# Optimization experiments

Measured on AMD Instinct MI355X. Metric: run time of the kernel, lower is better.

## Reference

```python
import jax, jax.numpy as jnp
import numpy as np

LMAX = 4
NC = (LMAX + 1) ** 2          # 25 spherical coefficients
L0 = LMAX + 1                 # number of m=0 coefficients
SPHERE = 128
CIN1 = 2 * SPHERE             # concat(source, target) channels
HID = 64
HEADS = 8
ALPHA_C = 64
VAL_C = 16
OUT_C = 128
GRID = 2 * (LMAX + 1)         # S2 grid resolution
N_NODES = 2500
N_EDGES = 25000
MAX_ELEM = 90
EDGE_IN = 128 + 2 * 64        # distance basis + src/tgt atom embeddings
M_SIZES = [LMAX - m + 1 for m in range(1, LMAX + 1)]  # l-count per |m|>0
RAD_OUT = L0 * CIN1 + sum(s * CIN1 for s in M_SIZES)  # 3840

def _lm(l, m):
    return l * l + l + m
_p = [_lm(l, 0) for l in range(LMAX + 1)]
for m in range(1, LMAX + 1):
    _p += [_lm(l, -m) for l in range(m, LMAX + 1)]
    _p += [_lm(l, m) for l in range(m, LMAX + 1)]
PERM = np.asarray(_p)             # l-primary -> m-primary
INV_PERM = np.argsort(PERM)       # m-primary -> l-primary
EXPAND = np.concatenate([np.full(2 * l + 1, l) for l in range(LMAX + 1)])

def _layernorm(x, g, b, eps=1e-5):
    mu = jnp.mean(x, axis=-1, keepdims=True)
    var = jnp.mean((x - mu) ** 2, axis=-1, keepdims=True)
    return (x - mu) * jax.lax.rsqrt(var + eps) * g + b

def _so2_conv(xm, fc0_w, fc0_b, wms, cin, mout, extra, rad):
    # xm: [E, NC, cin] in m-primary layout. Per-order SO(2) 'complex' conv.
    E = xm.shape[0]
    x0 = xm[:, :L0].reshape(E, L0 * cin)
    off_rad = L0 * cin
    if rad is not None:
        x0 = x0 * rad[:, :off_rad]
    x0 = x0 @ fc0_w + fc0_b
    x0_extra = None
    if extra:
        x0_extra = x0[:, :extra]
        x0 = x0[:, extra:]
    outs = [x0.reshape(E, L0, mout)]
    off = L0
    for i, sz in enumerate(M_SIZES):
        xb = xm[:, off:off + 2 * sz].reshape(E, 2, sz * cin)
        if rad is not None:
            xb = xb * rad[:, off_rad:off_rad + sz * cin][:, None, :]
            off_rad += sz * cin
        y = xb @ wms[i]                         # [E, 2, 2*mout*sz]
        half = y.shape[-1] // 2
        yr, yi = y[..., :half], y[..., half:]
        o = jnp.stack([yr[:, 0] - yi[:, 1], yr[:, 1] + yi[:, 0]], axis=1)
        outs.append(o.reshape(E, 2 * sz, mout))
        off += 2 * sz
    return jnp.concatenate(outs, axis=1), x0_extra

def _segment_softmax(logits, seg, num_segments):
    mx = jax.ops.segment_max(logits, seg, num_segments=num_segments)
    ex = jnp.exp(logits - mx[seg])
    s = jax.ops.segment_sum(ex, seg, num_segments=num_segments)
    return ex / (s[seg] + 1e-16)

def setup_inputs():
    key = jax.random.key(0)
    ks = iter(jax.random.split(key, 64))
    def nrm(shape, scale=1.0):
        return jax.random.normal(next(ks), shape, dtype=jnp.float32) * scale
    def lin(i, o):
        return nrm((i, o), i ** -0.5)
    inp = {}
    inp['x'] = nrm((N_NODES, NC, SPHERE))
    inp['edge_distance'] = nrm((N_EDGES, 128))
    inp['src_table'] = jax.random.uniform(next(ks), (MAX_ELEM, 64), jnp.float32, -0.001, 0.001)
    inp['tgt_table'] = jax.random.uniform(next(ks), (MAX_ELEM, 64), jnp.float32, -0.001, 0.001)
    inp['rad_w1'] = lin(EDGE_IN, 64); inp['rad_b1'] = jnp.zeros((64,), jnp.float32)
    inp['rad_ln1_g'] = jnp.ones((64,), jnp.float32); inp['rad_ln1_b'] = jnp.zeros((64,), jnp.float32)
    inp['rad_w2'] = lin(64, 64); inp['rad_b2'] = jnp.zeros((64,), jnp.float32)
    inp['rad_ln2_g'] = jnp.ones((64,), jnp.float32); inp['rad_ln2_b'] = jnp.zeros((64,), jnp.float32)
    inp['rad_w3'] = lin(64, RAD_OUT); inp['rad_b3'] = jnp.zeros((RAD_OUT,), jnp.float32)
    inp['wigner'] = nrm((N_EDGES, NC, NC), NC ** -0.5)
    extra1 = HEADS * ALPHA_C + HID
    inp['c1_fc0_w'] = lin(L0 * CIN1, L0 * HID + extra1)
    inp['c1_fc0_b'] = jnp.zeros((L0 * HID + extra1,), jnp.float32)
    for i, sz in enumerate(M_SIZES):
        inp['c1_wm%d' % (i + 1)] = lin(sz * CIN1, 2 * HID * sz)
    inp['to_grid'] = nrm((GRID, GRID, NC), NC ** -0.5)
    inp['from_grid'] = nrm((GRID, GRID, NC), float(GRID * GRID) ** -0.5)
    inp['alpha_ln_g'] = jnp.ones((ALPHA_C,), jnp.float32)
    inp['alpha_ln_b'] = jnp.zeros((ALPHA_C,), jnp.float32)
    std = ALPHA_C ** -0.5
    inp['alpha_dot'] = jax.random.uniform(next(ks), (HEADS, ALPHA_C), jnp.float32, -std, std)
    vout = HEADS * VAL_C
    inp['c2_fc0_w'] = lin(L0 * HID, L0 * vout)
    inp['c2_fc0_b'] = jnp.zeros((L0 * vout,), jnp.float32)
    for i, sz in enumerate(M_SIZES):
        inp['c2_wm%d' % (i + 1)] = lin(sz * HID, 2 * vout * sz)
    inp['proj_w'] = nrm((L0, OUT_C, vout), vout ** -0.5)
    inp['proj_b'] = jnp.zeros((OUT_C,), jnp.float32)
    inp['atomic_numbers'] = jax.random.randint(next(ks), (N_NODES,), 0, MAX_ELEM)
    inp['edge_index'] = jax.random.randint(next(ks), (2, N_EDGES), 0, N_NODES)
    return inp

def reference(x, edge_distance, src_table, tgt_table,
              rad_w1, rad_b1, rad_ln1_g, rad_ln1_b, rad_w2, rad_b2, rad_ln2_g, rad_ln2_b, rad_w3, rad_b3,
              wigner, c1_fc0_w, c1_fc0_b, c1_wm1, c1_wm2, c1_wm3, c1_wm4,
              to_grid, from_grid, alpha_ln_g, alpha_ln_b, alpha_dot,
              c2_fc0_w, c2_fc0_b, c2_wm1, c2_wm2, c2_wm3, c2_wm4, proj_w, proj_b,
              atomic_numbers, edge_index):
    E = edge_index.shape[1]
    N = x.shape[0]
    src, tgt = edge_index[0], edge_index[1]
    # invariant edge scalars: distance basis + source/target atom embeddings
    x_edge = jnp.concatenate([edge_distance, src_table[atomic_numbers[src]], tgt_table[atomic_numbers[tgt]]], axis=1)
    # gather node embeddings to edges, rotate into edge frame (Wigner-D)
    msg = jnp.concatenate([x[src], x[tgt]], axis=2)          # [E, NC, 2*SPHERE]
    msg = jnp.einsum('eml,elc->emc', wigner, msg)
    msg = msg[:, PERM]                                        # m-primary layout
    # radial MLP producing per-(m,l,channel) edge weights
    h = jax.nn.silu(_layernorm(x_edge @ rad_w1 + rad_b1, rad_ln1_g, rad_ln1_b))
    h = jax.nn.silu(_layernorm(h @ rad_w2 + rad_b2, rad_ln2_g, rad_ln2_b))
    rad = h @ rad_w3 + rad_b3                                 # [E, RAD_OUT]
    extra1 = HEADS * ALPHA_C + HID
    msg, x0_extra = _so2_conv(msg, c1_fc0_w, c1_fc0_b, (c1_wm1, c1_wm2, c1_wm3, c1_wm4), CIN1, HID, extra1, rad)
    x0_alpha = x0_extra[:, :HEADS * ALPHA_C]
    x0_gate = x0_extra[:, HEADS * ALPHA_C:]
    # separable S2 activation: scalar SiLU on l=0, grid SiLU on l>0
    msg_l = msg[:, INV_PERM]
    grid = jax.nn.silu(jnp.einsum('bai,eic->ebac', to_grid, msg_l))
    s2 = jnp.einsum('bai,ebac->eic', from_grid, grid)
    msg_l = jnp.concatenate([jax.nn.silu(x0_gate)[:, None, :], s2[:, 1:]], axis=1)
    # second SO(2) conv (internal weights, no radial)
    msg_m = msg_l[:, PERM]
    msg_m, _ = _so2_conv(msg_m, c2_fc0_w, c2_fc0_b, (c2_wm1, c2_wm2, c2_wm3, c2_wm4), HID, HEADS * VAL_C, None, None)
    msg_l = msg_m[:, INV_PERM]
    # attention logits (LayerNorm + SmoothLeakyReLU(0.2) + dot)
    a = _layernorm(x0_alpha.reshape(E, HEADS, ALPHA_C), alpha_ln_g, alpha_ln_b)
    a = 0.6 * a + 0.4 * a * (2.0 * jax.nn.sigmoid(a) - 1.0)
    logits = jnp.einsum('ehk,hk->eh', a, alpha_dot)
    # rotate messages back to global frame (wigner_inv = wigner^T)
    msg_l = jnp.einsum('eml,emc->elc', wigner, msg_l)
    alpha = _segment_softmax(logits, tgt, N)                  # [E, HEADS]
    v = msg_l.reshape(E, NC, HEADS, VAL_C) * alpha[:, None, :, None]
    node = jax.ops.segment_sum(v.reshape(E, NC, HEADS * VAL_C), tgt, num_segments=N)
    # SO3_LinearV2 projection: per-degree linear, bias only on l=0
    out = jnp.einsum('nmi,moi->nmo', node, proj_w[EXPAND])
    out = out.at[:, 0, :].add(proj_b)
    return out
```

## Files before the change

### kernel.cpp

```cpp
#include <hip/hip_runtime.h>
#include <cstddef>

typedef unsigned short u16;
typedef __attribute__((ext_vector_type(8))) short short8;
typedef __attribute__((ext_vector_type(4))) float float4v;

__constant__ int c_PERM[25] = {0,2,6,12,20, 1,5,11,19, 3,7,13,21, 4,10,18, 8,14,22, 9,17, 15,23, 16,24};
__constant__ int c_ROFF[25] = {0,256,512,768,1024, 1280,1536,1792,2048, 1280,1536,1792,2048,
                               2304,2560,2816, 2304,2560,2816, 3072,3328, 3072,3328, 3584,3584};
__constant__ int c_EXPAND[25] = {0,1,1,1,2,2,2,2,2,3,3,3,3,3,3,3,4,4,4,4,4,4,4,4,4};

static constexpr int PERM_CE[25] = {0,2,6,12,20, 1,5,11,19, 3,7,13,21, 4,10,18, 8,14,22, 9,17, 15,23, 16,24};
static constexpr int INV_CE[25]  = {0,5,1,9,13, 6,2,10,16,19, 14,7,3,11,17, 21,23,20,15,8, 4,12,18,22,24};

__device__ __forceinline__ float wsum64(float v){
#pragma unroll
  for(int m=32;m>0;m>>=1) v += __shfl_xor(v, m, 64);
  return v;
}
__device__ __forceinline__ float siluf(float x){ return x/(1.f+expf(-x)); }

__device__ __forceinline__ void bsplit(float v, u16 &h, u16 &l){
  unsigned u = __float_as_uint(v);
  unsigned hb = (u + 0x7FFFu + ((u>>16)&1u)) >> 16;
  h = (u16)hb;
  float r = v - __uint_as_float(hb<<16);
  unsigned u2 = __float_as_uint(r);
  l = (u16)((u2 + 0x7FFFu + ((u2>>16)&1u)) >> 16);
}

__global__ __launch_bounds__(256) void wtrans_kernel(const float* __restrict__ W, u16* __restrict__ Wh, u16* __restrict__ Wl, int K, int C2){
  int idx = blockIdx.x*256 + threadIdx.x;
  int K2 = 2*K;
  if(idx >= C2*K2) return;
  int n = idx / K2, k2 = idx % K2;
  int half = C2>>1;
  float v;
  if(k2 < K) v = W[k2*C2 + n];
  else { int k = k2-K; v = (n<half) ? -W[k*C2 + half + n] : W[k*C2 + n - half]; }
  u16 h,l; bsplit(v,h,l);
  Wh[idx]=h; Wl[idx]=l;
}

__global__ __launch_bounds__(256) void fctrans_kernel(const float* __restrict__ W, u16* __restrict__ Wh, u16* __restrict__ Wl, int K, int N){
  int idx = blockIdx.x*256 + threadIdx.x;
  if(idx >= N*K) return;
  int n = idx / K, k = idx % K;
  u16 h,l; bsplit(W[(size_t)k*N + n],h,l);
  Wh[idx]=h; Wl[idx]=l;
}

__global__ __launch_bounds__(256) void ptrans_kernel(const float* __restrict__ pw, float* __restrict__ pwt){
  int idx = blockIdx.x*256+threadIdx.x;
  if(idx >= 5*16384) return;
  int l = idx>>14, r = idx & 16383, i = r>>7, o = r&127;
  pwt[idx] = pw[(l<<14) + (o<<7) + i];
}

__global__ __launch_bounds__(64) void radial_kernel(
    const float* __restrict__ ed, const float* __restrict__ st, const float* __restrict__ tt,
    const float* __restrict__ w1, const float* __restrict__ b1, const float* __restrict__ g1, const float* __restrict__ bb1,
    const float* __restrict__ w2, const float* __restrict__ b2, const float* __restrict__ g2, const float* __restrict__ bb2,
    const int* __restrict__ an, const int* __restrict__ src, const int* __restrict__ tgt,
    u16* __restrict__ h2h, u16* __restrict__ h2l){
  int e = blockIdx.x; int lane = threadIdx.x;
  __shared__ float xe[256];
  __shared__ float h1s[64];
  int s = src[e], t = tgt[e];
  xe[lane]      = ed[(size_t)e*128 + lane];
  xe[64+lane]   = ed[(size_t)e*128 + 64 + lane];
  int as = an[s], at = an[t];
  xe[128+lane]  = st[as*64 + lane];
  xe[192+lane]  = tt[at*64 + lane];
  __syncthreads();
  float acc = b1[lane];
  for(int k=0;k<256;k++) acc += xe[k]*w1[k*64+lane];
  float mu = wsum64(acc)*(1.f/64.f);
  float d = acc - mu;
  float var = wsum64(d*d)*(1.f/64.f);
  float nrm = d*rsqrtf(var+1e-5f)*g1[lane]+bb1[lane];
  h1s[lane] = siluf(nrm);
  __syncthreads();
  float acc2 = b2[lane];
  for(int k=0;k<64;k++) acc2 += h1s[k]*w2[k*64+lane];
  mu = wsum64(acc2)*(1.f/64.f);
  d = acc2-mu;
  var = wsum64(d*d)*(1.f/64.f);
  nrm = d*rsqrtf(var+1e-5f)*g2[lane]+bb2[lane];
  u16 h,l; bsplit(siluf(nrm),h,l);
  h2h[(size_t)e*64+lane]=h; h2l[(size_t)e*64+lane]=l;
}

struct GrpArgs {
  const u16* Ah[6]; const u16* Al[6];
  const u16* Bh[6]; const u16* Bl[6];
  const float* bias[6]; float* C1[6]; float* C2[6];
  int lda[6]; int K[6]; int ldc1[6]; int ldc2[6]; int split[6];
  int xoff[7]; int ng; int M;
};

__global__ __launch_bounds__(256) void mgemm_kernel(GrpArgs a){
  __shared__ __align__(16) u16 Ash[128*40];
  __shared__ __align__(16) u16 Asl[128*40];
  __shared__ __align__(16) u16 Bsh[128*40];
  __shared__ __align__(16) u16 Bsl[128*40];
  int bx = blockIdx.x;
  int g = 0;
  while(g+1 < a.ng && bx >= a.xoff[g+1]) g++;
  int nx = bx - a.xoff[g];
  int n0 = nx*128, m0 = blockIdx.y*128;
  const int M = a.M, K = a.K[g], lda = a.lda[g];
  const u16* __restrict__ Ah = a.Ah[g]; const u16* __restrict__ Al = a.Al[g];
  const u16* __restrict__ Bh = a.Bh[g]; const u16* __restrict__ Bl = a.Bl[g];
  int t = threadIdx.x;
  int r0 = t>>2, k80 = (t&3)*8;
  int r1 = r0 + 64;
  int ar0 = m0 + r0; if(ar0 >= M) ar0 = M-1;
  int ar1 = m0 + r1; if(ar1 >= M) ar1 = M-1;
  const u16* Ap0h = Ah + (size_t)ar0*lda + k80;
  const u16* Ap1h = Ah + (size_t)ar1*lda + k80;
  const u16* Ap0l = Al + (size_t)ar0*lda + k80;
  const u16* Ap1l = Al + (size_t)ar1*lda + k80;
  const u16* Bp0h = Bh + (size_t)(n0+r0)*K + k80;
  const u16* Bp1h = Bh + (size_t)(n0+r1)*K + k80;
  const u16* Bp0l = Bl + (size_t)(n0+r0)*K + k80;
  const u16* Bp1l = Bl + (size_t)(n0+r1)*K + k80;
  int sA = r0*40 + k80;
  int sB = r1*40 + k80;

  int wave = t>>6, lane = t&63;
  int wr = wave>>1, wc = wave&1;
  int ml = lane&15, q = lane>>4;
  int aoff = (wr*64 + ml)*40 + q*8;
  int boff = (wc*64 + ml)*40 + q*8;

  float4v acc[4][4];
#pragma unroll
  for(int i=0;i<4;i++)
#pragma unroll
    for(int j=0;j<4;j++) acc[i][j] = 0.f;

  for(int k0=0; k0<K; k0+=32){
    short8 va0 = *(const short8*)(Ap0h + k0);
    short8 va1 = *(const short8*)(Ap1h + k0);
    short8 va2 = *(const short8*)(Ap0l + k0);
    short8 va3 = *(const short8*)(Ap1l + k0);
    short8 vb0 = *(const short8*)(Bp0h + k0);
    short8 vb1 = *(const short8*)(Bp1h + k0);
    short8 vb2 = *(const short8*)(Bp0l + k0);
    short8 vb3 = *(const short8*)(Bp1l + k0);
    __syncthreads();
    *(short8*)(Ash + sA) = va0;
    *(short8*)(Ash + sB) = va1;
    *(short8*)(Asl + sA) = va2;
    *(short8*)(Asl + sB) = va3;
    *(short8*)(Bsh + sA) = vb0;
    *(short8*)(Bsh + sB) = vb1;
    *(short8*)(Bsl + sA) = vb2;
    *(short8*)(Bsl + sB) = vb3;
    __syncthreads();
    short8 afh[4], afl[4], bfh[4], bfl[4];
#pragma unroll
    for(int i=0;i<4;i++){
      afh[i] = *(const short8*)(Ash + aoff + i*640);
      afl[i] = *(const short8*)(Asl + aoff + i*640);
      bfh[i] = *(const short8*)(Bsh + boff + i*640);
      bfl[i] = *(const short8*)(Bsl + boff + i*640);
    }
#pragma unroll
    for(int i=0;i<4;i++)
#pragma unroll
      for(int j=0;j<4;j++){
        acc[i][j] = __builtin_amdgcn_mfma_f32_16x16x32_bf16(afh[i], bfh[j], acc[i][j], 0,0,0);
        acc[i][j] = __builtin_amdgcn_mfma_f32_16x16x32_bf16(afh[i], bfl[j], acc[i][j], 0,0,0);
        acc[i][j] = __builtin_amdgcn_mfma_f32_16x16x32_bf16(afl[i], bfh[j], acc[i][j], 0,0,0);
      }
  }
  const float* bias = a.bias[g];
  int split = a.split[g];
  float* C1 = a.C1[g]; float* C2 = a.C2[g];
  int ldc1 = a.ldc1[g], ldc2 = a.ldc2[g];
#pragma unroll
  for(int i=0;i<4;i++){
    int rowb = m0 + wr*64 + i*16 + q*4;
#pragma unroll
    for(int r=0;r<4;r++){
      int row = rowb + r;
      if(row < M){
#pragma unroll
        for(int j=0;j<4;j++){
          int col = n0 + wc*64 + j*16 + ml;
          float v = acc[i][j][r];
          if(bias) v += bias[col];
          if(col < split) C1[(size_t)row*ldc1 + col] = v;
          else            C2[(size_t)row*ldc2 + (col-split)] = v;
        }
      }
    }
  }
}

__global__ __launch_bounds__(256) void wigner1_kernel(
    const float* __restrict__ x, const float* __restrict__ wigner,
    const int* __restrict__ src, const int* __restrict__ tgt,
    const float* __restrict__ rad, u16* __restrict__ msg1h, u16* __restrict__ msg1l){
  int e = blockIdx.x; int t = threadIdx.x;
  __shared__ float wig[625];
  __shared__ float4 cat4[1600];
  int s = src[e], tg = tgt[e];
  for(int i=t;i<625;i+=256) wig[i] = wigner[(size_t)e*625 + i];
  const float4* xs = (const float4*)(x + (size_t)s*3200);
  const float4* xt = (const float4*)(x + (size_t)tg*3200);
  for(int idx=t; idx<1600; idx+=256){
    int l = idx>>6, slot = idx&63;
    cat4[idx] = (slot<32) ? xs[l*32 + slot] : xt[l*32 + (slot-32)];
  }
  __syncthreads();
  int wave = t>>6, lane = t&63;
  for(int p=wave; p<25; p+=4){
    int pl = c_PERM[p];
    float4 acc = {0.f,0.f,0.f,0.f};
#pragma unroll
    for(int l=0;l<25;l++){
      float w = wig[pl*25 + l];
      float4 c = cat4[l*64 + lane];
      acc.x += w*c.x; acc.y += w*c.y; acc.z += w*c.z; acc.w += w*c.w;
    }
    float4 rd = *(const float4*)(rad + (size_t)e*3840 + c_ROFF[p] + lane*4);
    acc.x*=rd.x; acc.y*=rd.y; acc.z*=rd.z; acc.w*=rd.w;
    u16 h0,h1,h2,h3,l0,l1,l2,l3;
    bsplit(acc.x,h0,l0); bsplit(acc.y,h1,l1); bsplit(acc.z,h2,l2); bsplit(acc.w,h3,l3);
    size_t base = (size_t)e*6400 + p*256 + lane*4;
    *(uint2*)(msg1h + base) = make_uint2((unsigned)h0 | ((unsigned)h1<<16), (unsigned)h2 | ((unsigned)h3<<16));
    *(uint2*)(msg1l + base) = make_uint2((unsigned)l0 | ((unsigned)l1<<16), (unsigned)l2 | ((unsigned)l3<<16));
  }
}

__global__ __launch_bounds__(64) void grid_kernel(
    const float* __restrict__ msg2, const float* __restrict__ x0e,
    const float* __restrict__ tg, const float* __restrict__ fg,
    u16* __restrict__ m2h, u16* __restrict__ m2l){
  int e = blockIdx.x; int lane = threadIdx.x;
  float r[25];
#pragma unroll
  for(int i=0;i<25;i++) r[i] = msg2[((size_t)e*25 + INV_CE[i])*64 + lane];
  float s2[25];
#pragma unroll
  for(int i=0;i<25;i++) s2[i]=0.f;
  for(int g=0; g<100; g++){
    float tv=0.f;
#pragma unroll
    for(int i=0;i<25;i++) tv += tg[g*25+i]*r[i];
    tv = siluf(tv);
#pragma unroll
    for(int i=0;i<25;i++) s2[i] += fg[g*25+i]*tv;
  }
  float gate = siluf(x0e[(size_t)e*576 + 512 + lane]);
#pragma unroll
  for(int p=0;p<25;p++){
    int lp = PERM_CE[p];
    float v = (lp==0) ? gate : s2[lp];
    u16 h,l; bsplit(v,h,l);
    size_t idx = ((size_t)e*25+p)*64 + lane;
    m2h[idx]=h; m2l[idx]=l;
  }
}

__global__ __launch_bounds__(64) void alpha_kernel(
    const float* __restrict__ x0e, const float* __restrict__ g, const float* __restrict__ b,
    const float* __restrict__ adot, const int* __restrict__ tgt,
    float* __restrict__ exb, float* __restrict__ ssum){
  int e = blockIdx.x; int lane = threadIdx.x;
  int t = tgt[e];
  float gg = g[lane], bb = b[lane];
  for(int h=0;h<8;h++){
    float v = x0e[(size_t)e*576 + h*64 + lane];
    float mu = wsum64(v)*(1.f/64.f);
    float d = v-mu;
    float var = wsum64(d*d)*(1.f/64.f);
    float a = d*rsqrtf(var+1e-5f)*gg+bb;
    float sig = 1.f/(1.f+expf(-a));
    float a2 = 0.6f*a + 0.4f*a*(2.f*sig-1.f);
    float p = a2*adot[h*64+lane];
    float lg = wsum64(p);
    if(lane==0){
      float ex = expf(lg);
      exb[e*8+h]=ex;
      atomicAdd(&ssum[t*8+h], ex);
    }
  }
}

__global__ __launch_bounds__(256) void wigner2_kernel(
    const float* __restrict__ wigner, const float* __restrict__ msg3,
    const float* __restrict__ exb, const int* __restrict__ tgt,
    float* __restrict__ node){
  int e = blockIdx.x; int t = threadIdx.x;
  __shared__ float wig2[625];
  __shared__ float4 m3[800];
  __shared__ float al[8];
  int tg = tgt[e];
  for(int i=t;i<625;i+=256){ int q=i/25, l=i%25; wig2[i] = wigner[((size_t)e*25 + c_PERM[q])*25 + l]; }
  const float4* m3g = (const float4*)(msg3 + (size_t)e*3200);
  for(int i=t;i<800;i+=256) m3[i] = m3g[i];
  if(t<8) al[t] = exb[e*8+t];
  __syncthreads();
  int slot = t&31; int grp = t>>5;
  float* nb = node + (size_t)tg*3200;
  for(int l=grp; l<25; l+=8){
    float4 acc={0.f,0.f,0.f,0.f};
#pragma unroll
    for(int q=0;q<25;q++){
      float w = wig2[q*25+l];
      float4 m = m3[q*32+slot];
      acc.x+=w*m.x; acc.y+=w*m.y; acc.z+=w*m.z; acc.w+=w*m.w;
    }
    float a = al[slot>>2];
    int c = slot*4;
    atomicAdd(nb + l*128 + c+0, acc.x*a);
    atomicAdd(nb + l*128 + c+1, acc.y*a);
    atomicAdd(nb + l*128 + c+2, acc.z*a);
    atomicAdd(nb + l*128 + c+3, acc.w*a);
  }
}

__global__ __launch_bounds__(256) void proj_kernel(
    const float* __restrict__ node, const float* __restrict__ ssum,
    const float* __restrict__ pwt, const float* __restrict__ proj_b,
    float* __restrict__ out, int NN){
  int n0 = blockIdx.x*2; int t = threadIdx.x;
  __shared__ float nd[2][3200];
  __shared__ float inv[2][8];
  if(t<16){
    int j=t>>3, h=t&7;
    int n=n0+j; if(n>=NN) n=NN-1;
    inv[j][h] = 1.f/(ssum[n*8+h] + 1e-16f);
  }
  __syncthreads();
  int n1 = (n0+1 < NN) ? (n0+1) : (NN-1);
  for(int i=t;i<3200;i+=256){
    int h = (i&127)>>4;
    nd[0][i] = node[(size_t)n0*3200 + i] * inv[0][h];
    nd[1][i] = node[(size_t)n1*3200 + i] * inv[1][h];
  }
  __syncthreads();
  int o = t&127, half = t>>7;
  for(int p=half;p<25;p+=2){
    int l = c_EXPAND[p];
    const float* w = pwt + l*16384;
    float a0=0.f, a1=0.f;
    for(int i=0;i<128;i++){
      float wv = w[i*128+o];
      a0 += nd[0][p*128+i]*wv;
      a1 += nd[1][p*128+i]*wv;
    }
    float bs = (p==0)? proj_b[o] : 0.f;
    out[((size_t)n0*25+p)*128 + o] = a0 + bs;
    if(n0+1 < NN) out[((size_t)(n0+1)*25+p)*128 + o] = a1 + bs;
  }
}

extern "C" void kernel_launch(void* const* d_in, const int* in_sizes, int n_in,
                              void* d_out, int out_size, void* d_ws, size_t ws_size,
                              hipStream_t stream) {
  const float* x           = (const float*)d_in[0];
  const float* edge_dist   = (const float*)d_in[1];
  const float* src_table   = (const float*)d_in[2];
  const float* tgt_table   = (const float*)d_in[3];
  const float* rad_w1      = (const float*)d_in[4];
  const float* rad_b1      = (const float*)d_in[5];
  const float* rad_ln1_g   = (const float*)d_in[6];
  const float* rad_ln1_b   = (const float*)d_in[7];
  const float* rad_w2      = (const float*)d_in[8];
  const float* rad_b2      = (const float*)d_in[9];
  const float* rad_ln2_g   = (const float*)d_in[10];
  const float* rad_ln2_b   = (const float*)d_in[11];
  const float* rad_w3      = (const float*)d_in[12];
  const float* rad_b3      = (const float*)d_in[13];
  const float* wigner      = (const float*)d_in[14];
  const float* c1_fc0_w    = (const float*)d_in[15];
  const float* c1_fc0_b    = (const float*)d_in[16];
  const float* c1_wm[4]    = {(const float*)d_in[17],(const float*)d_in[18],(const float*)d_in[19],(const float*)d_in[20]};
  const float* to_grid     = (const float*)d_in[21];
  const float* from_grid   = (const float*)d_in[22];
  const float* alpha_ln_g  = (const float*)d_in[23];
  const float* alpha_ln_b  = (const float*)d_in[24];
  const float* alpha_dot   = (const float*)d_in[25];
  const float* c2_fc0_w    = (const float*)d_in[26];
  const float* c2_fc0_b    = (const float*)d_in[27];
  const float* c2_wm[4]    = {(const float*)d_in[28],(const float*)d_in[29],(const float*)d_in[30],(const float*)d_in[31]};
  const float* proj_w      = (const float*)d_in[32];
  const float* proj_b      = (const float*)d_in[33];
  const int*   atomic_nums = (const int*)d_in[34];
  const int*   edge_index  = (const int*)d_in[35];
  float* out = (float*)d_out;
  (void)n_in; (void)out_size;

  const int E  = in_sizes[35]/2;
  const int NN = in_sizes[34];

  const int K1[4] = {1024, 768, 512, 256}, C1c[4] = {512, 384, 256, 128};
  const int K2[4] = {256, 192, 128, 64},  C2c[4] = {1024, 768, 512, 256};
  const size_t W3T = 3840*64;
  const size_t FC1 = 896*1280;
  const size_t W1S[4] = {512*2048, 384*1536, 256*1024, 128*512};
  const size_t FC2 = 640*320;
  const size_t W2S[4] = {1024*512, 768*384, 512*256, 256*128};
  size_t wush = 2*(W3T + FC1 + W1S[0]+W1S[1]+W1S[2]+W1S[3] + FC2 + W2S[0]+W2S[1]+W2S[2]+W2S[3]);
  const size_t persist = (size_t)NN*8 + (size_t)NN*3200 + wush/2 + 81920 + 4096;
  const size_t wfl = ws_size / sizeof(float);
  const int copts[10] = {25000, 12500, 6250, 5000, 3125, 2500, 1250, 625, 250, 125};
  int C = 125;
  for(int i=0;i<10;i++){
    size_t need = (size_t)copts[i]*(6400+3840+576+8) + persist;
    if(need <= wfl){ C = copts[i]; break; }
  }

  float* ws = (float*)d_ws;
  u16* msg1h = (u16*)ws;
  u16* msg1l = msg1h + (size_t)C*6400;
  u16* m2h   = (u16*)ws;
  u16* m2l   = m2h + (size_t)C*1600;
  float* msg3 = ws + (size_t)C*1600;
  float* rad  = ws + (size_t)C*6400;
  float* msg2 = rad;
  float* x0e  = rad + (size_t)C*3840;
  u16* h2h = (u16*)x0e;
  u16* h2l = h2h + (size_t)C*64;
  float* exb  = x0e + (size_t)C*576;
  float* ssum = exb + (size_t)C*8;
  float* node = ssum + (size_t)NN*8;
  u16* wb = (u16*)(node + (size_t)NN*3200);
  u16 *w3h = wb, *w3l = w3h + W3T;
  u16 *f1h = w3l + W3T, *f1l = f1h + FC1;
  u16 *w1h[4], *w1l[4];
  u16* p = f1l + FC1;
  for(int i=0;i<4;i++){ w1h[i]=p; w1l[i]=p+W1S[i]; p += 2*W1S[i]; }
  u16 *f2h = p, *f2l = f2h + FC2; p = f2l + FC2;
  u16 *w2h[4], *w2l[4];
  for(int i=0;i<4;i++){ w2h[i]=p; w2l[i]=p+W2S[i]; p += 2*W2S[i]; }
  float* pwt = (float*)p;

  hipMemsetAsync(node, 0, (size_t)NN*3200*sizeof(float), stream);
  hipMemsetAsync(ssum, 0, (size_t)NN*8*sizeof(float), stream);

  fctrans_kernel<<<((int)W3T+255)/256, 256, 0, stream>>>(rad_w3, w3h, w3l, 64, 3840);
  fctrans_kernel<<<((int)FC1+255)/256, 256, 0, stream>>>(c1_fc0_w, f1h, f1l, 1280, 896);
  fctrans_kernel<<<((int)FC2+255)/256, 256, 0, stream>>>(c2_fc0_w, f2h, f2l, 320, 640);
  for(int i=0;i<4;i++)
    wtrans_kernel<<<((int)W1S[i]*2+255)/256, 256, 0, stream>>>(c1_wm[i], w1h[i], w1l[i], K1[i], C1c[i]);
  for(int i=0;i<4;i++)
    wtrans_kernel<<<((int)W2S[i]*2+255)/256, 256, 0, stream>>>(c2_wm[i], w2h[i], w2l[i], K2[i], C2c[i]);
  ptrans_kernel<<<320, 256, 0, stream>>>(proj_w, pwt);

  const int OFF1[4] = {5,13,19,23};
  int nch = (E + C - 1)/C;
  for(int ch=0; ch<nch; ch++){
    int e0 = ch*C;
    int ce = (E - e0 < C) ? (E - e0) : C;
    const int* srcp = edge_index + e0;
    const int* tgtp = edge_index + E + e0;
    const float* wigp = wigner + (size_t)e0*625;
    int mt = (ce+127)/128;

    radial_kernel<<<ce, 64, 0, stream>>>(edge_dist + (size_t)e0*128, src_table, tgt_table,
        rad_w1, rad_b1, rad_ln1_g, rad_ln1_b, rad_w2, rad_b2, rad_ln2_g, rad_ln2_b,
        atomic_nums, srcp, tgtp, h2h, h2l);

    {
      GrpArgs ga = {};
      ga.ng = 1; ga.M = ce;
      ga.Ah[0]=h2h; ga.Al[0]=h2l; ga.Bh[0]=w3h; ga.Bl[0]=w3l;
      ga.bias[0]=rad_b3; ga.C1[0]=rad; ga.C2[0]=nullptr;
      ga.lda[0]=64; ga.K[0]=64; ga.ldc1[0]=3840; ga.ldc2[0]=0; ga.split[0]=3840;
      ga.xoff[0]=0; ga.xoff[1]=30;
      mgemm_kernel<<<dim3(30, mt), 256, 0, stream>>>(ga);
    }

    wigner1_kernel<<<ce, 256, 0, stream>>>(x, wigp, srcp, tgtp, rad, msg1h, msg1l);

    {
      GrpArgs ga = {};
      ga.ng = 5; ga.M = ce;
      ga.Ah[0]=msg1h; ga.Al[0]=msg1l; ga.Bh[0]=f1h; ga.Bl[0]=f1l;
      ga.bias[0]=c1_fc0_b; ga.C1[0]=x0e; ga.C2[0]=msg2;
      ga.lda[0]=6400; ga.K[0]=1280; ga.ldc1[0]=576; ga.ldc2[0]=1600; ga.split[0]=576;
      int xo = 7;
      ga.xoff[0]=0; ga.xoff[1]=7;
      for(int i=0;i<4;i++){
        int gidx = i+1;
        ga.Ah[gidx]=msg1h + (size_t)OFF1[i]*256; ga.Al[gidx]=msg1l + (size_t)OFF1[i]*256;
        ga.Bh[gidx]=w1h[i]; ga.Bl[gidx]=w1l[i];
        ga.bias[gidx]=nullptr; ga.C1[gidx]=msg2 + OFF1[i]*64; ga.C2[gidx]=nullptr;
        ga.lda[gidx]=6400; ga.K[gidx]=2*K1[i]; ga.ldc1[gidx]=1600; ga.ldc2[gidx]=0; ga.split[gidx]=C1c[i];
        xo += C1c[i]/128;
        ga.xoff[gidx+1]=xo;
      }
      mgemm_kernel<<<dim3(xo, mt), 256, 0, stream>>>(ga);
    }

    grid_kernel<<<ce, 64, 0, stream>>>(msg2, x0e, to_grid, from_grid, m2h, m2l);
    alpha_kernel<<<ce, 64, 0, stream>>>(x0e, alpha_ln_g, alpha_ln_b, alpha_dot, tgtp, exb, ssum);

    {
      GrpArgs ga = {};
      ga.ng = 5; ga.M = ce;
      ga.Ah[0]=m2h; ga.Al[0]=m2l; ga.Bh[0]=f2h; ga.Bl[0]=f2l;
      ga.bias[0]=c2_fc0_b; ga.C1[0]=msg3; ga.C2[0]=nullptr;
      ga.lda[0]=1600; ga.K[0]=320; ga.ldc1[0]=3200; ga.ldc2[0]=0; ga.split[0]=640;
      int xo = 5;
      ga.xoff[0]=0; ga.xoff[1]=5;
      for(int i=0;i<4;i++){
        int gidx = i+1;
        ga.Ah[gidx]=m2h + (size_t)OFF1[i]*64; ga.Al[gidx]=m2l + (size_t)OFF1[i]*64;
        ga.Bh[gidx]=w2h[i]; ga.Bl[gidx]=w2l[i];
        ga.bias[gidx]=nullptr; ga.C1[gidx]=msg3 + OFF1[i]*128; ga.C2[gidx]=nullptr;
        ga.lda[gidx]=1600; ga.K[gidx]=2*K2[i]; ga.ldc1[gidx]=3200; ga.ldc2[gidx]=0; ga.split[gidx]=C2c[i];
        xo += C2c[i]/128;
        ga.xoff[gidx+1]=xo;
      }
      mgemm_kernel<<<dim3(xo, mt), 256, 0, stream>>>(ga);
    }

    wigner2_kernel<<<ce, 256, 0, stream>>>(wigp, msg3, exb, tgtp, node);
  }

  proj_kernel<<<(NN+1)/2, 256, 0, stream>>>(node, ssum, pwt, proj_b, out, NN);
}
```

Baseline: 4.071 ms.

## Replace atomic per-edge scatter with target-sorted per-node aggregation; prefetch GEMM tiles

Adds a counting sort of edges by target node for each chunk (histogram, scan and scatter kernels). The final rotate-and-scatter step now runs one block per node, walking that node's edges, accumulating in registers and writing each output row once, so the per-edge float atomicAdds into node memory go away. The grouped GEMM also now loads the next K-tile's global data into registers while MFMAs run on the current tile, and reorders the fragment loads. The cost is extra sort kernels, a grid sized by node count with uneven per-node work, and serialised per-edge loads inside each block.

```diff
diff --git a/kernel.cpp b/kernel.cpp
--- a/kernel.cpp
+++ b/kernel.cpp
@@ -55,6 +55,40 @@
   if(idx >= 5*16384) return;
   int l = idx>>14, r = idx & 16383, i = r>>7, o = r&127;
   pwt[idx] = pw[(l<<14) + (o<<7) + i];
+}
+
+__global__ __launch_bounds__(256) void hist_kernel(const int* __restrict__ tgt_all, int* __restrict__ cnt, int E, int C, int NN){
+  int idx = blockIdx.x*256+threadIdx.x;
+  if(idx>=E) return;
+  atomicAdd(&cnt[(idx/C)*NN + tgt_all[idx]], 1);
+}
+__global__ __launch_bounds__(256) void scan_kernel(const int* __restrict__ cnt, int* __restrict__ basearr, int* __restrict__ cur, int NN, int C){
+  int ch = blockIdx.x;
+  __shared__ int sh[256];
+  __shared__ int carry;
+  if(threadIdx.x==0) carry = ch*C;
+  __syncthreads();
+  for(int t0=0; t0<NN; t0+=256){
+    int i = t0 + threadIdx.x;
+    int v = (i<NN)? cnt[ch*NN+i] : 0;
+    sh[threadIdx.x]=v; __syncthreads();
+    for(int off=1; off<256; off<<=1){
+      int add = (threadIdx.x>=off)? sh[threadIdx.x-off]:0; __syncthreads();
+      sh[threadIdx.x]+=add; __syncthreads();
+    }
+    int excl = carry + sh[threadIdx.x]-v;
+    if(i<NN){ basearr[ch*NN+i]=excl; cur[ch*NN+i]=excl; }
+    __syncthreads();
+    if(threadIdx.x==255) carry += sh[255];
+    __syncthreads();
+  }
+}
+__global__ __launch_bounds__(256) void scatter_kernel(const int* __restrict__ tgt_all, int* __restrict__ cur, int* __restrict__ order, int E, int C, int NN){
+  int idx = blockIdx.x*256+threadIdx.x;
+  if(idx>=E) return;
+  int ch = idx / C;
+  int pos = atomicAdd(&cur[ch*NN + tgt_all[idx]], 1);
+  order[pos] = idx;
 }
 
 __global__ __launch_bounds__(64) void radial_kernel(
@@ -140,41 +174,53 @@
 #pragma unroll
     for(int j=0;j<4;j++) acc[i][j] = 0.f;
 
+  short8 cva[4], cvb[4];
+  cva[0] = *(const short8*)(Ap0h); cva[1] = *(const short8*)(Ap1h);
+  cva[2] = *(const short8*)(Ap0l); cva[3] = *(const short8*)(Ap1l);
+  cvb[0] = *(const short8*)(Bp0h); cvb[1] = *(const short8*)(Bp1h);
+  cvb[2] = *(const short8*)(Bp0l); cvb[3] = *(const short8*)(Bp1l);
+
   for(int k0=0; k0<K; k0+=32){
-    short8 va0 = *(const short8*)(Ap0h + k0);
-    short8 va1 = *(const short8*)(Ap1h + k0);
-    short8 va2 = *(const short8*)(Ap0l + k0);
-    short8 va3 = *(const short8*)(Ap1l + k0);
-    short8 vb0 = *(const short8*)(Bp0h + k0);
-    short8 vb1 = *(const short8*)(Bp1h + k0);
-    short8 vb2 = *(const short8*)(Bp0l + k0);
-    short8 vb3 = *(const short8*)(Bp1l + k0);
     __syncthreads();
-    *(short8*)(Ash + sA) = va0;
-    *(short8*)(Ash + sB) = va1;
-    *(short8*)(Asl + sA) = va2;
-    *(short8*)(Asl + sB) = va3;
-    *(short8*)(Bsh + sA) = vb0;
-    *(short8*)(Bsh + sB) = vb1;
-    *(short8*)(Bsl + sA) = vb2;
-    *(short8*)(Bsl + sB) = vb3;
+    *(short8*)(Ash + sA) = cva[0];
+    *(short8*)(Ash + sB) = cva[1];
+    *(short8*)(Asl + sA) = cva[2];
+    *(short8*)(Asl + sB) = cva[3];
+    *(short8*)(Bsh + sA) = cvb[0];
+    *(short8*)(Bsh + sB) = cvb[1];
+    *(short8*)(Bsl + sA) = cvb[2];
+    *(short8*)(Bsl + sB) = cvb[3];
     __syncthreads();
-    short8 afh[4], afl[4], bfh[4], bfl[4];
+    short8 nva[4], nvb[4];
+    bool more = (k0+32 < K);
+    if(more){
+      int kn = k0+32;
+      nva[0] = *(const short8*)(Ap0h + kn); nva[1] = *(const short8*)(Ap1h + kn);
+      nva[2] = *(const short8*)(Ap0l + kn); nva[3] = *(const short8*)(Ap1l + kn);
+      nvb[0] = *(const short8*)(Bp0h + kn); nvb[1] = *(const short8*)(Bp1h + kn);
+      nvb[2] = *(const short8*)(Bp0l + kn); nvb[3] = *(const short8*)(Bp1l + kn);
+    }
+    short8 afh[4], afl[4];
 #pragma unroll
     for(int i=0;i<4;i++){
       afh[i] = *(const short8*)(Ash + aoff + i*640);
       afl[i] = *(const short8*)(Asl + aoff + i*640);
-      bfh[i] = *(const short8*)(Bsh + boff + i*640);
-      bfl[i] = *(const short8*)(Bsl + boff + i*640);
-    }
-#pragma unroll
-    for(int i=0;i<4;i++)
-#pragma unroll
-      for(int j=0;j<4;j++){
-        acc[i][j] = __builtin_amdgcn_mfma_f32_16x16x32_bf16(afh[i], bfh[j], acc[i][j], 0,0,0);
-        acc[i][j] = __builtin_amdgcn_mfma_f32_16x16x32_bf16(afh[i], bfl[j], acc[i][j], 0,0,0);
-        acc[i][j] = __builtin_amdgcn_mfma_f32_16x16x32_bf16(afl[i], bfh[j], acc[i][j], 0,0,0);
+    }
+#pragma unroll
+    for(int j=0;j<4;j++){
+      short8 bfh = *(const short8*)(Bsh + boff + j*640);
+      short8 bfl = *(const short8*)(Bsl + boff + j*640);
+#pragma unroll
+      for(int i=0;i<4;i++){
+        acc[i][j] = __builtin_amdgcn_mfma_f32_16x16x32_bf16(afh[i], bfh, acc[i][j], 0,0,0);
+        acc[i][j] = __builtin_amdgcn_mfma_f32_16x16x32_bf16(afh[i], bfl, acc[i][j], 0,0,0);
+        acc[i][j] = __builtin_amdgcn_mfma_f32_16x16x32_bf16(afl[i], bfh, acc[i][j], 0,0,0);
       }
+    }
+    if(more){
+#pragma unroll
+      for(int i=0;i<4;i++){ cva[i]=nva[i]; cvb[i]=nvb[i]; }
+    }
   }
   const float* bias = a.bias[g];
   int split = a.split[g];
@@ -291,37 +337,48 @@
   }
 }
 
-__global__ __launch_bounds__(256) void wigner2_kernel(
-    const float* __restrict__ wigner, const float* __restrict__ msg3,
-    const float* __restrict__ exb, const int* __restrict__ tgt,
-    float* __restrict__ node){
-  int e = blockIdx.x; int t = threadIdx.x;
+__global__ __launch_bounds__(256) void agg_kernel(
+    const float* __restrict__ wigner_all, const float* __restrict__ msg3,
+    const float* __restrict__ exb, const int* __restrict__ order,
+    const int* __restrict__ basearr, const int* __restrict__ cnt,
+    float* __restrict__ node, int e0){
+  int n = blockIdx.x; int t = threadIdx.x;
+  int lg = t>>5;
+  int c4 = t&31;
   __shared__ float wig2[625];
-  __shared__ float4 m3[800];
-  __shared__ float al[8];
-  int tg = tgt[e];
-  for(int i=t;i<625;i+=256){ int q=i/25, l=i%25; wig2[i] = wigner[((size_t)e*25 + c_PERM[q])*25 + l]; }
-  const float4* m3g = (const float4*)(msg3 + (size_t)e*3200);
-  for(int i=t;i<800;i+=256) m3[i] = m3g[i];
-  if(t<8) al[t] = exb[e*8+t];
-  __syncthreads();
-  int slot = t&31; int grp = t>>5;
-  float* nb = node + (size_t)tg*3200;
-  for(int l=grp; l<25; l+=8){
-    float4 acc={0.f,0.f,0.f,0.f};
-#pragma unroll
+  __shared__ float m3s[3200];
+  float4v acc[4];
+#pragma unroll
+  for(int k=0;k<4;k++) acc[k] = 0.f;
+  float* nb = node + (size_t)n*3200;
+#pragma unroll
+  for(int k=0;k<4;k++){ int l = lg + 8*k; if(l<25) acc[k] = *(const float4v*)(nb + l*128 + c4*4); }
+  int nE = cnt[n], b0 = basearr[n];
+  for(int j=0;j<nE;j++){
+    int e = order[b0+j];
+    int el = e - e0;
+    __syncthreads();
+    for(int i=t;i<625;i+=256){ int q=i/25, l=i%25; wig2[i] = wigner_all[((size_t)e*25 + c_PERM[q])*25 + l]; }
+    for(int i=t;i<800;i+=256) ((float4*)m3s)[i] = ((const float4*)(msg3 + (size_t)el*3200))[i];
+    __syncthreads();
+    float ex = exb[el*8 + (c4>>2)];
+    float4v tmp[4];
+#pragma unroll
+    for(int k=0;k<4;k++) tmp[k] = 0.f;
     for(int q=0;q<25;q++){
-      float w = wig2[q*25+l];
-      float4 m = m3[q*32+slot];
-      acc.x+=w*m.x; acc.y+=w*m.y; acc.z+=w*m.z; acc.w+=w*m.w;
-    }
-    float a = al[slot>>2];
-    int c = slot*4;
-    atomicAdd(nb + l*128 + c+0, acc.x*a);
-    atomicAdd(nb + l*128 + c+1, acc.y*a);
-    atomicAdd(nb + l*128 + c+2, acc.z*a);
-    atomicAdd(nb + l*128 + c+3, acc.w*a);
-  }
+      float4v m = *(const float4v*)(m3s + q*128 + c4*4);
+#pragma unroll
+      for(int k=0;k<4;k++){
+        int l = lg + 8*k;
+        float w = (l<25) ? wig2[q*25 + l] : 0.f;
+        tmp[k] += w*m;
+      }
+    }
+#pragma unroll
+    for(int k=0;k<4;k++) acc[k] += ex*tmp[k];
+  }
+#pragma unroll
+  for(int k=0;k<4;k++){ int l = lg + 8*k; if(l<25) *(float4v*)(nb + l*128 + c4*4) = acc[k]; }
 }
 
 __global__ __launch_bounds__(256) void proj_kernel(
@@ -412,9 +469,11 @@
   const int copts[10] = {25000, 12500, 6250, 5000, 3125, 2500, 1250, 625, 250, 125};
   int C = 125;
   for(int i=0;i<10;i++){
-    size_t need = (size_t)copts[i]*(6400+3840+576+8) + persist;
+    size_t nchI = (size_t)((E + copts[i]-1)/copts[i]);
+    size_t need = (size_t)copts[i]*(6400+3840+576+8) + persist + 3*nchI*NN + E;
     if(need <= wfl){ C = copts[i]; break; }
   }
+  const int nch = (E + C - 1)/C;
 
   float* ws = (float*)d_ws;
   u16* msg1h = (u16*)ws;
@@ -440,9 +499,19 @@
   u16 *w2h[4], *w2l[4];
   for(int i=0;i<4;i++){ w2h[i]=p; w2l[i]=p+W2S[i]; p += 2*W2S[i]; }
   float* pwt = (float*)p;
+  int* cntb  = (int*)(pwt + 81920);
+  int* baseb = cntb + (size_t)nch*NN;
+  int* curb  = baseb + (size_t)nch*NN;
+  int* order = curb + (size_t)nch*NN;
 
   hipMemsetAsync(node, 0, (size_t)NN*3200*sizeof(float), stream);
   hipMemsetAsync(ssum, 0, (size_t)NN*8*sizeof(float), stream);
+  hipMemsetAsync(cntb, 0, (size_t)nch*NN*sizeof(int), stream);
+
+  const int* tgt_all = edge_index + E;
+  hist_kernel<<<(E+255)/256, 256, 0, stream>>>(tgt_all, cntb, E, C, NN);
+  scan_kernel<<<nch, 256, 0, stream>>>(cntb, baseb, curb, NN, C);
+  scatter_kernel<<<(E+255)/256, 256, 0, stream>>>(tgt_all, curb, order, E, C, NN);
 
   fctrans_kernel<<<((int)W3T+255)/256, 256, 0, stream>>>(rad_w3, w3h, w3l, 64, 3840);
   fctrans_kernel<<<((int)FC1+255)/256, 256, 0, stream>>>(c1_fc0_w, f1h, f1l, 1280, 896);
@@ -454,7 +523,6 @@
   ptrans_kernel<<<320, 256, 0, stream>>>(proj_w, pwt);
 
   const int OFF1[4] = {5,13,19,23};
-  int nch = (E + C - 1)/C;
   for(int ch=0; ch<nch; ch++){
     int e0 = ch*C;
     int ce = (E - e0 < C) ? (E - e0) : C;
@@ -522,7 +590,8 @@
       mgemm_kernel<<<dim3(xo, mt), 256, 0, stream>>>(ga);
     }
 
-    wigner2_kernel<<<ce, 256, 0, stream>>>(wigp, msg3, exb, tgtp, node);
+    agg_kernel<<<NN, 256, 0, stream>>>(wigner, msg3, exb, order,
+        baseb + (size_t)ch*NN, cntb + (size_t)ch*NN, node, e0);
   }
 
   proj_kernel<<<(NN+1)/2, 256, 0, stream>>>(node, ssum, pwt, proj_b, out, NN);
```

After: 3.661 ms. 10.1% less time.
